# Performance work log

Hardware: AMD Instinct MI355X
Metric: run time of the kernel (lower is better)

The kernel has to match this reference:

```python
import math
import jax, jax.numpy as jnp
import numpy as np

DIM = 1024
HEADS = 16
HEAD_DIM = DIM // HEADS
NEG = -10000.0


def setup_inputs() -> dict:
    key = jax.random.key(0)
    ks = jax.random.split(key, 9)
    B, S = 2, 2048
    s = 1.0 / math.sqrt(DIM)
    inp = {
        "x": jax.random.normal(ks[0], (B, S, DIM), dtype=jnp.float32),
        "Wq": jax.random.normal(ks[1], (DIM, DIM), dtype=jnp.float32) * s,
        "bq": jnp.zeros((DIM,), dtype=jnp.float32),
        "Wk": jax.random.normal(ks[2], (DIM, DIM), dtype=jnp.float32) * s,
        "bk": jnp.zeros((DIM,), dtype=jnp.float32),
        "Wv": jax.random.normal(ks[3], (DIM, DIM), dtype=jnp.float32) * s,
        "bv": jnp.zeros((DIM,), dtype=jnp.float32),
        "Wo": jax.random.normal(ks[4], (DIM, DIM), dtype=jnp.float32) * s,
        "bo": jnp.zeros((DIM,), dtype=jnp.float32),
    }
    return inp


def reference(x, Wq, bq, Wk, bk, Wv, bv, Wo, bo):
    B, S, D = x.shape
    q = x @ Wq + bq
    k = x @ Wk + bk
    v = x @ Wv + bv
    # [B, H, S, hd]
    def split_heads(t):
        return t.reshape(B, S, HEADS, HEAD_DIM).transpose(0, 2, 1, 3)
    q, k, v = split_heads(q), split_heads(k), split_heads(v)
    scores = jnp.einsum("bhqd,bhkd->bhqk", q, k) / math.sqrt(HEAD_DIM)
    causal = jnp.tril(jnp.ones((S, S), dtype=bool))  # [S, S]
    scores = jnp.where(causal[None, None], scores, NEG)
    probs = jax.nn.softmax(scores, axis=-1)
    ctx = jnp.einsum("bhqk,bhkd->bhqd", probs, v)  # [B, H, S, hd]
    ctx = ctx.transpose(0, 2, 1, 3).reshape(B, S, D)
    out = ctx @ Wo + bo
    return out
```

## Files before the change

kernel.cpp:

```cpp
#include <hip/hip_runtime.h>
#include <hip/hip_bf16.h>
#include <math.h>

#define DIMX 1024
#define HEADSX 16
#define HDX 64
#define BBX 2
#define SSX 2048
#define MMX (BBX*SSX)

typedef __bf16 bf16x8 __attribute__((ext_vector_type(8)));
typedef __bf16 bf16x4 __attribute__((ext_vector_type(4)));
typedef float  f32x4  __attribute__((ext_vector_type(4)));

#define NEGF (-1e30f)
#define QSCALE 0.18033688011112042f

template<bool B> struct BoolC { static constexpr bool value = B; };

static __device__ __forceinline__ void gload16(const void* g, void* l) {
  __builtin_amdgcn_global_load_lds(
      (const __attribute__((address_space(1))) unsigned int*)g,
      (__attribute__((address_space(3))) unsigned int*)l, 16, 0, 0);
}

__global__ __launch_bounds__(256) void k_prep(
    const float* __restrict__ x, const float* __restrict__ Wq,
    const float* __restrict__ Wk, const float* __restrict__ Wv,
    const float* __restrict__ Wo, __bf16* __restrict__ xb,
    __bf16* __restrict__ wqkvT, __bf16* __restrict__ woT) {
  const int bid = blockIdx.x;
  if (bid < 4096) {
    int i = (bid * 256 + threadIdx.x) * 4;
    float4 v = *(const float4*)&x[i];
    bf16x4 o = { (__bf16)v.x, (__bf16)v.y, (__bf16)v.z, (__bf16)v.w };
    *(bf16x4*)&xb[i] = o;
    return;
  }
  __shared__ __bf16 tile[64][65];
  const int wb = bid - 4096;
  const int mat = wb >> 8, t8 = wb & 255;
  const float* src = (mat == 0) ? Wq : (mat == 1) ? Wk : (mat == 2) ? Wv : Wo;
  __bf16* dst = (mat < 3) ? (wqkvT + (size_t)mat * DIMX * DIMX) : woT;
  const int tx = t8 & 15, ty = t8 >> 4;
  const int k0 = ty * 64, n0 = tx * 64;
  #pragma unroll
  for (int rep = 0; rep < 16; ++rep) {
    int idx = rep * 256 + threadIdx.x;
    int r = idx >> 6, c = idx & 63;
    tile[r][c] = (__bf16)src[(size_t)(k0 + r) * DIMX + n0 + c];
  }
  __syncthreads();
  #pragma unroll
  for (int rep = 0; rep < 16; ++rep) {
    int idx = rep * 256 + threadIdx.x;
    int r = idx >> 6, c = idx & 63;
    dst[(size_t)(n0 + r) * DIMX + k0 + c] = tile[c][r];
  }
}

__global__ __launch_bounds__(256) void k_gemm_qkv(
    const __bf16* __restrict__ A,
    const __bf16* __restrict__ Bt,
    const float* __restrict__ b0, const float* __restrict__ b1,
    const float* __restrict__ b2,
    __bf16* __restrict__ qb, __bf16* __restrict__ kb, __bf16* __restrict__ vtb) {
  constexpr int BK = 32, K = 1024;
  __shared__ __bf16 As[128 * BK];
  __shared__ __bf16 Bs[128 * BK];
  const int tid = threadIdx.x, lane = tid & 63, wave = tid >> 6;
  const int g = lane >> 4, r16 = lane & 15;
  const int wm = wave & 1, wn = wave >> 1;
  const int id = blockIdx.x;
  const int xcd = id & 7, j96 = id >> 3;
  const int m0 = (xcd * 4 + (j96 & 3)) * 128;
  const int n0 = (j96 >> 2) * 128;

  f32x4 acc[4][4] = {};

  for (int k0 = 0; k0 < K; k0 += BK) {
    __syncthreads();
    #pragma unroll
    for (int i = 0; i < 2; ++i) {
      int c = wave * 64 + lane + 256 * i;
      gload16(&A [(size_t)(m0 + (c >> 2)) * K + k0 + (c & 3) * 8],
              (char*)As + (size_t)(wave * 64 + 256 * i) * 16);
      gload16(&Bt[(size_t)(n0 + (c >> 2)) * K + k0 + (c & 3) * 8],
              (char*)Bs + (size_t)(wave * 64 + 256 * i) * 16);
    }
    __syncthreads();
    bf16x8 af[4], bfr[4];
    #pragma unroll
    for (int i = 0; i < 4; ++i)
      af[i]  = *(const bf16x8*)&As[(wm * 64 + i * 16 + r16) * BK + g * 8];
    #pragma unroll
    for (int j = 0; j < 4; ++j)
      bfr[j] = *(const bf16x8*)&Bs[(wn * 64 + j * 16 + r16) * BK + g * 8];
    #pragma unroll
    for (int i = 0; i < 4; ++i)
      #pragma unroll
      for (int j = 0; j < 4; ++j)
        acc[i][j] = __builtin_amdgcn_mfma_f32_16x16x32_bf16(af[i], bfr[j],
                                                            acc[i][j], 0, 0, 0);
  }

  #pragma unroll
  for (int i = 0; i < 4; ++i) {
    #pragma unroll
    for (int j = 0; j < 4; ++j) {
      #pragma unroll
      for (int r = 0; r < 4; ++r) {
        int m = m0 + wm * 64 + i * 16 + 4 * g + r;
        int n = n0 + wn * 64 + j * 16 + r16;
        float v = acc[i][j][r];
        int proj = n >> 10, w = n & 1023, h = w >> 6, d = w & 63;
        const float* bp = (proj == 0) ? b0 : (proj == 1) ? b1 : b2;
        v += bp[w];
        int b = m >> 11, s = m & 2047, bh = b * HEADSX + h;
        if (proj == 0)      qb [((size_t)bh * SSX + s) * HDX + d] =
                                (__bf16)(v * QSCALE);
        else if (proj == 1) kb [((size_t)bh * SSX + s) * HDX + d] = (__bf16)v;
        else                vtb[((size_t)bh * HDX + d) * SSX + s] = (__bf16)v;
      }
    }
  }
}

__global__ __launch_bounds__(256) void k_gemm_out(
    const __bf16* __restrict__ A,
    const __bf16* __restrict__ Bt,
    const float* __restrict__ bias, float* __restrict__ outf) {
  constexpr int BK = 32, K = 1024;
  __shared__ __bf16 As[128 * BK];
  __shared__ __bf16 Bs[64 * BK];
  const int tid = threadIdx.x, lane = tid & 63, wave = tid >> 6;
  const int g = lane >> 4, r16 = lane & 15;
  const int wm = wave & 1, wn = wave >> 1;
  const int id = blockIdx.x;
  const int xcd = id & 7, j64 = id >> 3;
  const int m0 = (xcd * 4 + (j64 & 3)) * 128;
  const int n0 = (j64 >> 2) * 64;

  f32x4 acc[4][2] = {};

  for (int k0 = 0; k0 < K; k0 += BK) {
    __syncthreads();
    #pragma unroll
    for (int i = 0; i < 2; ++i) {
      int c = wave * 64 + lane + 256 * i;
      gload16(&A [(size_t)(m0 + (c >> 2)) * K + k0 + (c & 3) * 8],
              (char*)As + (size_t)(wave * 64 + 256 * i) * 16);
    }
    {
      int c = tid;
      gload16(&Bt[(size_t)(n0 + (c >> 2)) * K + k0 + (c & 3) * 8],
              (char*)Bs + (size_t)(wave * 64) * 16);
    }
    __syncthreads();
    bf16x8 af[4], bfr[2];
    #pragma unroll
    for (int i = 0; i < 4; ++i)
      af[i]  = *(const bf16x8*)&As[(wm * 64 + i * 16 + r16) * BK + g * 8];
    #pragma unroll
    for (int j = 0; j < 2; ++j)
      bfr[j] = *(const bf16x8*)&Bs[(wn * 32 + j * 16 + r16) * BK + g * 8];
    #pragma unroll
    for (int i = 0; i < 4; ++i)
      #pragma unroll
      for (int j = 0; j < 2; ++j)
        acc[i][j] = __builtin_amdgcn_mfma_f32_16x16x32_bf16(af[i], bfr[j],
                                                            acc[i][j], 0, 0, 0);
  }

  #pragma unroll
  for (int i = 0; i < 4; ++i)
    #pragma unroll
    for (int j = 0; j < 2; ++j)
      #pragma unroll
      for (int r = 0; r < 4; ++r) {
        int m = m0 + wm * 64 + i * 16 + 4 * g + r;
        int n = n0 + wn * 32 + j * 16 + r16;
        outf[(size_t)m * DIMX + n] = acc[i][j][r] + bias[n];
      }
}

__global__ __launch_bounds__(256, 2) void k_attn(
    const __bf16* __restrict__ qb, const __bf16* __restrict__ kb,
    const __bf16* __restrict__ vtb, __bf16* __restrict__ ctxb) {
  const int tid = threadIdx.x;
  const int lane = tid & 63, wq = tid >> 6;
  const int g = lane >> 4, r16 = lane & 15;

  const int id = blockIdx.x;
  const int xcd = id & 7, idx = id >> 3;
  const int bh = xcd * 4 + (idx & 3);
  const int p  = idx >> 2;
  const int b = bh >> 4, h = bh & 15;

  const int ntL = p + 1, ntH = 32 - p;
  const int q0L = p * 64 + wq * 16;
  const int q0H = (31 - p) * 64 + wq * 16;

  const __bf16* Q  = qb  + (size_t)bh * SSX * HDX;
  const __bf16* Kp = kb  + (size_t)bh * SSX * HDX;
  const __bf16* Vt = vtb + (size_t)bh * HDX * SSX;

  __shared__ __bf16 Ks[2][64 * 64];
  __shared__ __bf16 Vs[2][64 * 64];
  __shared__ unsigned Pld[8][512];

  bf16x8 qfL[2], qfH[2];
  qfL[0] = *(const bf16x8*)&Q[(size_t)(q0L + r16) * HDX + g * 8];
  qfL[1] = *(const bf16x8*)&Q[(size_t)(q0L + r16) * HDX + 32 + g * 8];
  qfH[0] = *(const bf16x8*)&Q[(size_t)(q0H + r16) * HDX + g * 8];
  qfH[1] = *(const bf16x8*)&Q[(size_t)(q0H + r16) * HDX + 32 + g * 8];

  f32x4 accL[4] = {}, accH[4] = {};
  float mrunL = NEGF, lrunL = 0.f;
  float mrunH = NEGF, lrunH = 0.f;

  auto STAGE = [&](int buf, int t) {
    const int kv0 = t * 64;
    #pragma unroll
    for (int i = 0; i < 2; ++i) {
      int c = tid + 256 * i;
      int r = c >> 3;
      int cb = (c & 7) ^ (r & 7);
      gload16(&Kp[(size_t)(kv0 + r) * HDX + cb * 8],
              (char*)Ks[buf] + (size_t)(wq * 64 + 256 * i) * 16);
      gload16(&Vt[(size_t)r * SSX + kv0 + cb * 8],
              (char*)Vs[buf] + (size_t)(wq * 64 + 256 * i) * 16);
    }
  };

  auto SM = [&](f32x4* sac, f32x4* acc, float& mrun, float& lrun,
                int qrow, bool last, int kv0, unsigned* pld) {
    float pv[4][4];
    float mt = NEGF;
    #pragma unroll
    for (int jj = 0; jj < 4; ++jj)
      #pragma unroll
      for (int r = 0; r < 4; ++r) {
        float s = sac[jj][r];
        if (last) {
          int kcol = kv0 + jj * 16 + 4 * g + r;
          s = (kcol > qrow) ? NEGF : s;
        }
        pv[jj][r] = s;
        mt = fmaxf(mt, s);
      }
    mt = fmaxf(mt, __shfl_xor(mt, 16));
    mt = fmaxf(mt, __shfl_xor(mt, 32));
    if (__any(mt > mrun)) {
      float mnew = fmaxf(mrun, mt);
      float fac = exp2f(mrun - mnew);
      mrun = mnew;
      lrun *= fac;
      #pragma unroll
      for (int j2 = 0; j2 < 4; ++j2)
        #pragma unroll
        for (int r = 0; r < 4; ++r)
          acc[j2][r] *= fac;
    }
    float rs = 0.f;
    #pragma unroll
    for (int jj = 0; jj < 4; ++jj)
      #pragma unroll
      for (int r = 0; r < 4; ++r) {
        float px = exp2f(pv[jj][r] - mrun);
        pv[jj][r] = px;
        rs += px;
      }
    lrun += rs;
    #pragma unroll
    for (int jj = 0; jj < 4; ++jj)
      #pragma unroll
      for (int rp = 0; rp < 2; ++rp) {
        unsigned w;
        asm("v_cvt_pk_bf16_f32 %0, %1, %2"
            : "=v"(w) : "v"(pv[jj][2 * rp]), "v"(pv[jj][2 * rp + 1]));
        int c = jj * 8 + g * 2 + rp;
        int addr = r16 * 32 + (((c >> 2) ^ (r16 & 7)) << 2) + (c & 3);
        pld[addr] = w;
      }
  };

  auto STEP = [&](auto dolc, int t, bool lastH) {
    constexpr bool doL = decltype(dolc)::value;
    const int cur = t & 1;
    if (t + 1 < ntH) STAGE(cur ^ 1, t + 1);
    const int kv0 = t * 64;

    f32x4 sacH[4] = {}, sacL[4] = {};
    __builtin_amdgcn_s_setprio(1);
    #pragma unroll
    for (int kk = 0; kk < 2; ++kk)
      #pragma unroll
      for (int jj = 0; jj < 4; ++jj) {
        int rr = jj * 16 + r16;
        bf16x8 kf = *(const bf16x8*)
            &Ks[cur][rr * 64 + (((kk << 2) + g) ^ (rr & 7)) * 8];
        sacH[jj] = __builtin_amdgcn_mfma_f32_16x16x32_bf16(kf, qfH[kk],
                                                           sacH[jj], 0, 0, 0);
        if constexpr (doL)
          sacL[jj] = __builtin_amdgcn_mfma_f32_16x16x32_bf16(kf, qfL[kk],
                                                             sacL[jj], 0, 0, 0);
      }
    __builtin_amdgcn_s_setprio(0);

    SM(sacH, accH, mrunH, lrunH, q0H + r16, lastH, kv0, &Pld[wq * 2][0]);
    if constexpr (doL)
      SM(sacL, accL, mrunL, lrunL, q0L + r16, t == ntL - 1, kv0,
         &Pld[wq * 2 + 1][0]);

    bf16x8 pfH[2], pfL[2];
    #pragma unroll
    for (int half = 0; half < 2; ++half) {
      int c = half * 16 + g * 4;
      int addr = r16 * 32 + (((c >> 2) ^ (r16 & 7)) << 2);
      pfH[half] = *(const bf16x8*)&Pld[wq * 2][addr];
      if constexpr (doL) pfL[half] = *(const bf16x8*)&Pld[wq * 2 + 1][addr];
    }
    __builtin_amdgcn_s_setprio(1);
    #pragma unroll
    for (int j2 = 0; j2 < 4; ++j2)
      #pragma unroll
      for (int half = 0; half < 2; ++half) {
        int dd = j2 * 16 + r16;
        bf16x8 vf = *(const bf16x8*)
            &Vs[cur][dd * 64 + (((half << 2) + g) ^ (dd & 7)) * 8];
        accH[j2] = __builtin_amdgcn_mfma_f32_16x16x32_bf16(vf, pfH[half],
                                                           accH[j2], 0, 0, 0);
        if constexpr (doL)
          accL[j2] = __builtin_amdgcn_mfma_f32_16x16x32_bf16(vf, pfL[half],
                                                             accL[j2], 0, 0, 0);
      }
    __builtin_amdgcn_s_setprio(0);
  };

  STAGE(0, 0);
  __syncthreads();

  int t = 0;
  for (; t < ntL; ++t) {
    STEP(BoolC<true>{}, t, false);
    __syncthreads();
  }
  for (; t < ntH; ++t) {
    STEP(BoolC<false>{}, t, t == ntH - 1);
    __syncthreads();
  }

  auto EPIL = [&](f32x4* acc, float lrun, int q0) {
    lrun += __shfl_xor(lrun, 16);
    lrun += __shfl_xor(lrun, 32);
    const float inv = 1.f / lrun;
    const int s = q0 + r16;
    #pragma unroll
    for (int j2 = 0; j2 < 4; ++j2)
      #pragma unroll
      for (int r = 0; r < 4; ++r) {
        int d = j2 * 16 + 4 * g + r;
        ctxb[((size_t)(b * SSX + s)) * DIMX + h * HDX + d] =
            (__bf16)(acc[j2][r] * inv);
      }
  };
  EPIL(accH, lrunH, q0H);
  EPIL(accL, lrunL, q0L);
}

extern "C" void kernel_launch(void* const* d_in, const int* in_sizes, int n_in,
                              void* d_out, int out_size, void* d_ws,
                              size_t ws_size, hipStream_t stream) {
  const float* x  = (const float*)d_in[0];
  const float* Wq = (const float*)d_in[1];
  const float* bq = (const float*)d_in[2];
  const float* Wk = (const float*)d_in[3];
  const float* bk = (const float*)d_in[4];
  const float* Wv = (const float*)d_in[5];
  const float* bv = (const float*)d_in[6];
  const float* Wo = (const float*)d_in[7];
  const float* bo = (const float*)d_in[8];
  float* out = (float*)d_out;

  char* ws = (char*)d_ws;
  __bf16* xb    = (__bf16*)(ws);
  __bf16* wqkvT = (__bf16*)(ws + ((size_t)8  << 20));
  __bf16* woT   = (__bf16*)(ws + ((size_t)14 << 20));
  __bf16* qb    = (__bf16*)(ws + ((size_t)16 << 20));
  __bf16* kb    = (__bf16*)(ws + ((size_t)24 << 20));
  __bf16* vtb   = (__bf16*)(ws + ((size_t)32 << 20));
  __bf16* ctxb  = xb;

  k_prep<<<5120, 256, 0, stream>>>(x, Wq, Wk, Wv, Wo, xb, wqkvT, woT);
  k_gemm_qkv<<<768, 256, 0, stream>>>(xb, wqkvT, bq, bk, bv, qb, kb, vtb);
  k_attn<<<512, 256, 0, stream>>>(qb, kb, vtb, ctxb);
  k_gemm_out<<<512, 256, 0, stream>>>(ctxb, woT, bo, out);
}
```

Before: 117.5 us.

## Split attention low/high query tiles across 8 waves and widen GEMM K-tile

The attention kernel now runs 512 threads per block. Waves 0-3 handle the high (long) query tile and waves 4-7 handle the paired low tile, so each wave holds one accumulator set instead of two. This lowers register pressure and raises parallelism, at the cost of the low-tile waves idling at barriers once their shorter causal range is done. Both GEMMs move to BK=64 with XOR-swizzled LDS layouts, which halves the barrier count per K loop and avoids bank conflicts.

```diff
diff --git a/kernel.cpp b/kernel.cpp
--- a/kernel.cpp
+++ b/kernel.cpp
@@ -15,8 +15,6 @@
 
 #define NEGF (-1e30f)
 #define QSCALE 0.18033688011112042f
-
-template<bool B> struct BoolC { static constexpr bool value = B; };
 
 static __device__ __forceinline__ void gload16(const void* g, void* l) {
   __builtin_amdgcn_global_load_lds(
@@ -65,7 +63,7 @@
     const float* __restrict__ b0, const float* __restrict__ b1,
     const float* __restrict__ b2,
     __bf16* __restrict__ qb, __bf16* __restrict__ kb, __bf16* __restrict__ vtb) {
-  constexpr int BK = 32, K = 1024;
+  constexpr int BK = 64, K = 1024;
   __shared__ __bf16 As[128 * BK];
   __shared__ __bf16 Bs[128 * BK];
   const int tid = threadIdx.x, lane = tid & 63, wave = tid >> 6;
@@ -81,27 +79,35 @@
   for (int k0 = 0; k0 < K; k0 += BK) {
     __syncthreads();
     #pragma unroll
-    for (int i = 0; i < 2; ++i) {
-      int c = wave * 64 + lane + 256 * i;
-      gload16(&A [(size_t)(m0 + (c >> 2)) * K + k0 + (c & 3) * 8],
+    for (int i = 0; i < 4; ++i) {
+      int c = tid + 256 * i;
+      int r = c >> 3, cb = (c & 7) ^ (r & 7);
+      gload16(&A [(size_t)(m0 + r) * K + k0 + cb * 8],
               (char*)As + (size_t)(wave * 64 + 256 * i) * 16);
-      gload16(&Bt[(size_t)(n0 + (c >> 2)) * K + k0 + (c & 3) * 8],
+      gload16(&Bt[(size_t)(n0 + r) * K + k0 + cb * 8],
               (char*)Bs + (size_t)(wave * 64 + 256 * i) * 16);
     }
     __syncthreads();
-    bf16x8 af[4], bfr[4];
-    #pragma unroll
-    for (int i = 0; i < 4; ++i)
-      af[i]  = *(const bf16x8*)&As[(wm * 64 + i * 16 + r16) * BK + g * 8];
-    #pragma unroll
-    for (int j = 0; j < 4; ++j)
-      bfr[j] = *(const bf16x8*)&Bs[(wn * 64 + j * 16 + r16) * BK + g * 8];
-    #pragma unroll
-    for (int i = 0; i < 4; ++i)
-      #pragma unroll
-      for (int j = 0; j < 4; ++j)
-        acc[i][j] = __builtin_amdgcn_mfma_f32_16x16x32_bf16(af[i], bfr[j],
-                                                            acc[i][j], 0, 0, 0);
+    #pragma unroll
+    for (int kk = 0; kk < 2; ++kk) {
+      bf16x8 af[4], bfr[4];
+      #pragma unroll
+      for (int i = 0; i < 4; ++i) {
+        int rr = wm * 64 + i * 16 + r16;
+        af[i] = *(const bf16x8*)&As[rr * 64 + (((kk << 2) + g) ^ (rr & 7)) * 8];
+      }
+      #pragma unroll
+      for (int j = 0; j < 4; ++j) {
+        int rn = wn * 64 + j * 16 + r16;
+        bfr[j] = *(const bf16x8*)&Bs[rn * 64 + (((kk << 2) + g) ^ (rn & 7)) * 8];
+      }
+      #pragma unroll
+      for (int i = 0; i < 4; ++i)
+        #pragma unroll
+        for (int j = 0; j < 4; ++j)
+          acc[i][j] = __builtin_amdgcn_mfma_f32_16x16x32_bf16(af[i], bfr[j],
+                                                              acc[i][j], 0, 0, 0);
+    }
   }
 
   #pragma unroll
@@ -130,7 +136,7 @@
     const __bf16* __restrict__ A,
     const __bf16* __restrict__ Bt,
     const float* __restrict__ bias, float* __restrict__ outf) {
-  constexpr int BK = 32, K = 1024;
+  constexpr int BK = 64, K = 1024;
   __shared__ __bf16 As[128 * BK];
   __shared__ __bf16 Bs[64 * BK];
   const int tid = threadIdx.x, lane = tid & 63, wave = tid >> 6;
@@ -146,30 +152,40 @@
   for (int k0 = 0; k0 < K; k0 += BK) {
     __syncthreads();
     #pragma unroll
+    for (int i = 0; i < 4; ++i) {
+      int c = tid + 256 * i;
+      int r = c >> 3, cb = (c & 7) ^ (r & 7);
+      gload16(&A[(size_t)(m0 + r) * K + k0 + cb * 8],
+              (char*)As + (size_t)(wave * 64 + 256 * i) * 16);
+    }
+    #pragma unroll
     for (int i = 0; i < 2; ++i) {
-      int c = wave * 64 + lane + 256 * i;
-      gload16(&A [(size_t)(m0 + (c >> 2)) * K + k0 + (c & 3) * 8],
-              (char*)As + (size_t)(wave * 64 + 256 * i) * 16);
-    }
-    {
-      int c = tid;
-      gload16(&Bt[(size_t)(n0 + (c >> 2)) * K + k0 + (c & 3) * 8],
-              (char*)Bs + (size_t)(wave * 64) * 16);
-    }
-    __syncthreads();
-    bf16x8 af[4], bfr[2];
-    #pragma unroll
-    for (int i = 0; i < 4; ++i)
-      af[i]  = *(const bf16x8*)&As[(wm * 64 + i * 16 + r16) * BK + g * 8];
-    #pragma unroll
-    for (int j = 0; j < 2; ++j)
-      bfr[j] = *(const bf16x8*)&Bs[(wn * 32 + j * 16 + r16) * BK + g * 8];
-    #pragma unroll
-    for (int i = 0; i < 4; ++i)
-      #pragma unroll
-      for (int j = 0; j < 2; ++j)
-        acc[i][j] = __builtin_amdgcn_mfma_f32_16x16x32_bf16(af[i], bfr[j],
-                                                            acc[i][j], 0, 0, 0);
+      int c = tid + 256 * i;
+      int r = c >> 3, cb = (c & 7) ^ (r & 7);
+      gload16(&Bt[(size_t)(n0 + r) * K + k0 + cb * 8],
+              (char*)Bs + (size_t)(wave * 64 + 256 * i) * 16);
+    }
+    __syncthreads();
+    #pragma unroll
+    for (int kk = 0; kk < 2; ++kk) {
+      bf16x8 af[4], bfr[2];
+      #pragma unroll
+      for (int i = 0; i < 4; ++i) {
+        int rr = wm * 64 + i * 16 + r16;
+        af[i] = *(const bf16x8*)&As[rr * 64 + (((kk << 2) + g) ^ (rr & 7)) * 8];
+      }
+      #pragma unroll
+      for (int j = 0; j < 2; ++j) {
+        int rn = wn * 32 + j * 16 + r16;
+        bfr[j] = *(const bf16x8*)&Bs[rn * 64 + (((kk << 2) + g) ^ (rn & 7)) * 8];
+      }
+      #pragma unroll
+      for (int i = 0; i < 4; ++i)
+        #pragma unroll
+        for (int j = 0; j < 2; ++j)
+          acc[i][j] = __builtin_amdgcn_mfma_f32_16x16x32_bf16(af[i], bfr[j],
+                                                              acc[i][j], 0, 0, 0);
+    }
   }
 
   #pragma unroll
@@ -184,7 +200,7 @@
       }
 }
 
-__global__ __launch_bounds__(256, 2) void k_attn(
+__global__ __launch_bounds__(512, 4) void k_attn(
     const __bf16* __restrict__ qb, const __bf16* __restrict__ kb,
     const __bf16* __restrict__ vtb, __bf16* __restrict__ ctxb) {
   const int tid = threadIdx.x;
@@ -198,8 +214,10 @@
   const int b = bh >> 4, h = bh & 15;
 
   const int ntL = p + 1, ntH = 32 - p;
-  const int q0L = p * 64 + wq * 16;
-  const int q0H = (31 - p) * 64 + wq * 16;
+  const bool isH = (wq < 4);
+  const int myNt = isH ? ntH : ntL;
+  const int q0 = isH ? ((31 - p) * 64 + wq * 16)
+                     : (p * 64 + (wq - 4) * 16);
 
   const __bf16* Q  = qb  + (size_t)bh * SSX * HDX;
   const __bf16* Kp = kb  + (size_t)bh * SSX * HDX;
@@ -209,164 +227,135 @@
   __shared__ __bf16 Vs[2][64 * 64];
   __shared__ unsigned Pld[8][512];
 
-  bf16x8 qfL[2], qfH[2];
-  qfL[0] = *(const bf16x8*)&Q[(size_t)(q0L + r16) * HDX + g * 8];
-  qfL[1] = *(const bf16x8*)&Q[(size_t)(q0L + r16) * HDX + 32 + g * 8];
-  qfH[0] = *(const bf16x8*)&Q[(size_t)(q0H + r16) * HDX + g * 8];
-  qfH[1] = *(const bf16x8*)&Q[(size_t)(q0H + r16) * HDX + 32 + g * 8];
-
-  f32x4 accL[4] = {}, accH[4] = {};
-  float mrunL = NEGF, lrunL = 0.f;
-  float mrunH = NEGF, lrunH = 0.f;
+  bf16x8 qf[2];
+  qf[0] = *(const bf16x8*)&Q[(size_t)(q0 + r16) * HDX + g * 8];
+  qf[1] = *(const bf16x8*)&Q[(size_t)(q0 + r16) * HDX + 32 + g * 8];
+
+  f32x4 acc[4] = {};
+  float mrun = NEGF, lrun = 0.f;
+  const int qrow = q0 + r16;
 
   auto STAGE = [&](int buf, int t) {
     const int kv0 = t * 64;
-    #pragma unroll
-    for (int i = 0; i < 2; ++i) {
-      int c = tid + 256 * i;
-      int r = c >> 3;
-      int cb = (c & 7) ^ (r & 7);
-      gload16(&Kp[(size_t)(kv0 + r) * HDX + cb * 8],
-              (char*)Ks[buf] + (size_t)(wq * 64 + 256 * i) * 16);
-      gload16(&Vt[(size_t)r * SSX + kv0 + cb * 8],
-              (char*)Vs[buf] + (size_t)(wq * 64 + 256 * i) * 16);
-    }
+    int c = tid;
+    int r = c >> 3;
+    int cb = (c & 7) ^ (r & 7);
+    gload16(&Kp[(size_t)(kv0 + r) * HDX + cb * 8],
+            (char*)Ks[buf] + (size_t)(wq * 64) * 16);
+    gload16(&Vt[(size_t)r * SSX + kv0 + cb * 8],
+            (char*)Vs[buf] + (size_t)(wq * 64) * 16);
   };
 
-  auto SM = [&](f32x4* sac, f32x4* acc, float& mrun, float& lrun,
-                int qrow, bool last, int kv0, unsigned* pld) {
-    float pv[4][4];
-    float mt = NEGF;
-    #pragma unroll
-    for (int jj = 0; jj < 4; ++jj)
-      #pragma unroll
-      for (int r = 0; r < 4; ++r) {
-        float s = sac[jj][r];
-        if (last) {
-          int kcol = kv0 + jj * 16 + 4 * g + r;
-          s = (kcol > qrow) ? NEGF : s;
-        }
-        pv[jj][r] = s;
-        mt = fmaxf(mt, s);
-      }
-    mt = fmaxf(mt, __shfl_xor(mt, 16));
-    mt = fmaxf(mt, __shfl_xor(mt, 32));
-    if (__any(mt > mrun)) {
-      float mnew = fmaxf(mrun, mt);
-      float fac = exp2f(mrun - mnew);
-      mrun = mnew;
-      lrun *= fac;
-      #pragma unroll
-      for (int j2 = 0; j2 < 4; ++j2)
-        #pragma unroll
-        for (int r = 0; r < 4; ++r)
-          acc[j2][r] *= fac;
-    }
-    float rs = 0.f;
-    #pragma unroll
-    for (int jj = 0; jj < 4; ++jj)
-      #pragma unroll
-      for (int r = 0; r < 4; ++r) {
-        float px = exp2f(pv[jj][r] - mrun);
-        pv[jj][r] = px;
-        rs += px;
-      }
-    lrun += rs;
-    #pragma unroll
-    for (int jj = 0; jj < 4; ++jj)
-      #pragma unroll
-      for (int rp = 0; rp < 2; ++rp) {
-        unsigned w;
-        asm("v_cvt_pk_bf16_f32 %0, %1, %2"
-            : "=v"(w) : "v"(pv[jj][2 * rp]), "v"(pv[jj][2 * rp + 1]));
-        int c = jj * 8 + g * 2 + rp;
-        int addr = r16 * 32 + (((c >> 2) ^ (r16 & 7)) << 2) + (c & 3);
-        pld[addr] = w;
-      }
-  };
-
-  auto STEP = [&](auto dolc, int t, bool lastH) {
-    constexpr bool doL = decltype(dolc)::value;
+  STAGE(0, 0);
+  __syncthreads();
+
+  for (int t = 0; t < ntH; ++t) {
     const int cur = t & 1;
     if (t + 1 < ntH) STAGE(cur ^ 1, t + 1);
-    const int kv0 = t * 64;
-
-    f32x4 sacH[4] = {}, sacL[4] = {};
-    __builtin_amdgcn_s_setprio(1);
-    #pragma unroll
-    for (int kk = 0; kk < 2; ++kk)
-      #pragma unroll
-      for (int jj = 0; jj < 4; ++jj) {
-        int rr = jj * 16 + r16;
-        bf16x8 kf = *(const bf16x8*)
-            &Ks[cur][rr * 64 + (((kk << 2) + g) ^ (rr & 7)) * 8];
-        sacH[jj] = __builtin_amdgcn_mfma_f32_16x16x32_bf16(kf, qfH[kk],
-                                                           sacH[jj], 0, 0, 0);
-        if constexpr (doL)
-          sacL[jj] = __builtin_amdgcn_mfma_f32_16x16x32_bf16(kf, qfL[kk],
-                                                             sacL[jj], 0, 0, 0);
-      }
-    __builtin_amdgcn_s_setprio(0);
-
-    SM(sacH, accH, mrunH, lrunH, q0H + r16, lastH, kv0, &Pld[wq * 2][0]);
-    if constexpr (doL)
-      SM(sacL, accL, mrunL, lrunL, q0L + r16, t == ntL - 1, kv0,
-         &Pld[wq * 2 + 1][0]);
-
-    bf16x8 pfH[2], pfL[2];
-    #pragma unroll
-    for (int half = 0; half < 2; ++half) {
-      int c = half * 16 + g * 4;
-      int addr = r16 * 32 + (((c >> 2) ^ (r16 & 7)) << 2);
-      pfH[half] = *(const bf16x8*)&Pld[wq * 2][addr];
-      if constexpr (doL) pfL[half] = *(const bf16x8*)&Pld[wq * 2 + 1][addr];
-    }
-    __builtin_amdgcn_s_setprio(1);
-    #pragma unroll
-    for (int j2 = 0; j2 < 4; ++j2)
+    if (t < myNt) {
+      const int kv0 = t * 64;
+      const bool last = (t == myNt - 1);
+
+      f32x4 sac[4] = {};
+      __builtin_amdgcn_s_setprio(1);
+      #pragma unroll
+      for (int kk = 0; kk < 2; ++kk)
+        #pragma unroll
+        for (int jj = 0; jj < 4; ++jj) {
+          int rr = jj * 16 + r16;
+          bf16x8 kf = *(const bf16x8*)
+              &Ks[cur][rr * 64 + (((kk << 2) + g) ^ (rr & 7)) * 8];
+          sac[jj] = __builtin_amdgcn_mfma_f32_16x16x32_bf16(kf, qf[kk],
+                                                            sac[jj], 0, 0, 0);
+        }
+      __builtin_amdgcn_s_setprio(0);
+
+      float pv[4][4];
+      float mt = NEGF;
+      #pragma unroll
+      for (int jj = 0; jj < 4; ++jj)
+        #pragma unroll
+        for (int r = 0; r < 4; ++r) {
+          float s = sac[jj][r];
+          if (last) {
+            int kcol = kv0 + jj * 16 + 4 * g + r;
+            s = (kcol > qrow) ? NEGF : s;
+          }
+          pv[jj][r] = s;
+          mt = fmaxf(mt, s);
+        }
+      mt = fmaxf(mt, __shfl_xor(mt, 16));
+      mt = fmaxf(mt, __shfl_xor(mt, 32));
+
+      if (__any(mt > mrun)) {
+        float mnew = fmaxf(mrun, mt);
+        float fac = exp2f(mrun - mnew);
+        mrun = mnew;
+        lrun *= fac;
+        #pragma unroll
+        for (int j2 = 0; j2 < 4; ++j2)
+          #pragma unroll
+          for (int r = 0; r < 4; ++r)
+            acc[j2][r] *= fac;
+      }
+      float rs = 0.f;
+      #pragma unroll
+      for (int jj = 0; jj < 4; ++jj)
+        #pragma unroll
+        for (int r = 0; r < 4; ++r) {
+          float px = exp2f(pv[jj][r] - mrun);
+          pv[jj][r] = px;
+          rs += px;
+        }
+      lrun += rs;
+
+      #pragma unroll
+      for (int jj = 0; jj < 4; ++jj)
+        #pragma unroll
+        for (int rp = 0; rp < 2; ++rp) {
+          unsigned w;
+          asm("v_cvt_pk_bf16_f32 %0, %1, %2"
+              : "=v"(w) : "v"(pv[jj][2 * rp]), "v"(pv[jj][2 * rp + 1]));
+          int c = jj * 8 + g * 2 + rp;
+          int addr = r16 * 32 + (((c >> 2) ^ (r16 & 7)) << 2) + (c & 3);
+          Pld[wq][addr] = w;
+        }
+
+      bf16x8 pf[2];
       #pragma unroll
       for (int half = 0; half < 2; ++half) {
-        int dd = j2 * 16 + r16;
-        bf16x8 vf = *(const bf16x8*)
-            &Vs[cur][dd * 64 + (((half << 2) + g) ^ (dd & 7)) * 8];
-        accH[j2] = __builtin_amdgcn_mfma_f32_16x16x32_bf16(vf, pfH[half],
-                                                           accH[j2], 0, 0, 0);
-        if constexpr (doL)
-          accL[j2] = __builtin_amdgcn_mfma_f32_16x16x32_bf16(vf, pfL[half],
-                                                             accL[j2], 0, 0, 0);
-      }
-    __builtin_amdgcn_s_setprio(0);
-  };
-
-  STAGE(0, 0);
-  __syncthreads();
-
-  int t = 0;
-  for (; t < ntL; ++t) {
-    STEP(BoolC<true>{}, t, false);
-    __syncthreads();
-  }
-  for (; t < ntH; ++t) {
-    STEP(BoolC<false>{}, t, t == ntH - 1);
-    __syncthreads();
-  }
-
-  auto EPIL = [&](f32x4* acc, float lrun, int q0) {
-    lrun += __shfl_xor(lrun, 16);
-    lrun += __shfl_xor(lrun, 32);
-    const float inv = 1.f / lrun;
-    const int s = q0 + r16;
-    #pragma unroll
-    for (int j2 = 0; j2 < 4; ++j2)
-      #pragma unroll
-      for (int r = 0; r < 4; ++r) {
-        int d = j2 * 16 + 4 * g + r;
-        ctxb[((size_t)(b * SSX + s)) * DIMX + h * HDX + d] =
-            (__bf16)(acc[j2][r] * inv);
-      }
-  };
-  EPIL(accH, lrunH, q0H);
-  EPIL(accL, lrunL, q0L);
+        int c = half * 16 + g * 4;
+        int addr = r16 * 32 + (((c >> 2) ^ (r16 & 7)) << 2);
+        pf[half] = *(const bf16x8*)&Pld[wq][addr];
+      }
+      __builtin_amdgcn_s_setprio(1);
+      #pragma unroll
+      for (int j2 = 0; j2 < 4; ++j2)
+        #pragma unroll
+        for (int half = 0; half < 2; ++half) {
+          int dd = j2 * 16 + r16;
+          bf16x8 vf = *(const bf16x8*)
+              &Vs[cur][dd * 64 + (((half << 2) + g) ^ (dd & 7)) * 8];
+          acc[j2] = __builtin_amdgcn_mfma_f32_16x16x32_bf16(vf, pf[half],
+                                                            acc[j2], 0, 0, 0);
+        }
+      __builtin_amdgcn_s_setprio(0);
+    }
+    __syncthreads();
+  }
+
+  lrun += __shfl_xor(lrun, 16);
+  lrun += __shfl_xor(lrun, 32);
+  const float inv = 1.f / lrun;
+  const int s = q0 + r16;
+  #pragma unroll
+  for (int j2 = 0; j2 < 4; ++j2)
+    #pragma unroll
+    for (int r = 0; r < 4; ++r) {
+      int d = j2 * 16 + 4 * g + r;
+      ctxb[((size_t)(b * SSX + s)) * DIMX + h * HDX + d] =
+          (__bf16)(acc[j2][r] * inv);
+    }
 }
 
 extern "C" void kernel_launch(void* const* d_in, const int* in_sizes, int n_in,
@@ -394,6 +383,6 @@
 
   k_prep<<<5120, 256, 0, stream>>>(x, Wq, Wk, Wv, Wo, xb, wqkvT, woT);
   k_gemm_qkv<<<768, 256, 0, stream>>>(xb, wqkvT, bq, bk, bv, qb, kb, vtb);
-  k_attn<<<512, 256, 0, stream>>>(qb, kb, vtb, ctxb);
+  k_attn<<<512, 512, 0, stream>>>(qb, kb, vtb, ctxb);
   k_gemm_out<<<512, 256, 0, stream>>>(ctxb, woT, bo, out);
 }
```

After: 128.5 us. +9.4%, slower.

## Process two KV tiles per barrier with four-slot LDS ring buffer

Applied to the files above, without the earlier changes.

The attention loop now stages K/V into a four-slot LDS ring and handles two 64-key tiles per iteration, so there is one __syncthreads per two tiles and prefetch runs two tiles ahead. The interleaved low/high query-tile MFMA issue is replaced by sequential per-subtile processing that shares one P scratch buffer per wave. This cuts barrier count and increases load lookahead, at the cost of doubling K/V LDS use (fewer resident blocks) and losing the interleaving of independent L/H MFMA chains.

```diff
diff --git a/kernel.cpp b/kernel.cpp
--- a/kernel.cpp
+++ b/kernel.cpp
@@ -15,8 +15,6 @@
 
 #define NEGF (-1e30f)
 #define QSCALE 0.18033688011112042f
-
-template<bool B> struct BoolC { static constexpr bool value = B; };
 
 static __device__ __forceinline__ void gload16(const void* g, void* l) {
   __builtin_amdgcn_global_load_lds(
@@ -205,9 +203,9 @@
   const __bf16* Kp = kb  + (size_t)bh * SSX * HDX;
   const __bf16* Vt = vtb + (size_t)bh * HDX * SSX;
 
-  __shared__ __bf16 Ks[2][64 * 64];
-  __shared__ __bf16 Vs[2][64 * 64];
-  __shared__ unsigned Pld[8][512];
+  __shared__ __bf16 Ks[4][64 * 64];
+  __shared__ __bf16 Vs[4][64 * 64];
+  __shared__ unsigned Pld[4][512];
 
   bf16x8 qfL[2], qfH[2];
   qfL[0] = *(const bf16x8*)&Q[(size_t)(q0L + r16) * HDX + g * 8];
@@ -219,7 +217,8 @@
   float mrunL = NEGF, lrunL = 0.f;
   float mrunH = NEGF, lrunH = 0.f;
 
-  auto STAGE = [&](int buf, int t) {
+  auto STAGE = [&](int t) {
+    const int slot = t & 3;
     const int kv0 = t * 64;
     #pragma unroll
     for (int i = 0; i < 2; ++i) {
@@ -227,14 +226,28 @@
       int r = c >> 3;
       int cb = (c & 7) ^ (r & 7);
       gload16(&Kp[(size_t)(kv0 + r) * HDX + cb * 8],
-              (char*)Ks[buf] + (size_t)(wq * 64 + 256 * i) * 16);
+              (char*)Ks[slot] + (size_t)(wq * 64 + 256 * i) * 16);
       gload16(&Vt[(size_t)r * SSX + kv0 + cb * 8],
-              (char*)Vs[buf] + (size_t)(wq * 64 + 256 * i) * 16);
+              (char*)Vs[slot] + (size_t)(wq * 64 + 256 * i) * 16);
     }
   };
 
-  auto SM = [&](f32x4* sac, f32x4* acc, float& mrun, float& lrun,
-                int qrow, bool last, int kv0, unsigned* pld) {
+  auto SUBTILE = [&](const bf16x8* qf, f32x4* acc, float& mrun, float& lrun,
+                     int qrow, bool last, int kv0, int slot) {
+    f32x4 sac[4] = {};
+    __builtin_amdgcn_s_setprio(1);
+    #pragma unroll
+    for (int kk = 0; kk < 2; ++kk)
+      #pragma unroll
+      for (int jj = 0; jj < 4; ++jj) {
+        int rr = jj * 16 + r16;
+        bf16x8 kf = *(const bf16x8*)
+            &Ks[slot][rr * 64 + (((kk << 2) + g) ^ (rr & 7)) * 8];
+        sac[jj] = __builtin_amdgcn_mfma_f32_16x16x32_bf16(kf, qf[kk], sac[jj],
+                                                          0, 0, 0);
+      }
+    __builtin_amdgcn_s_setprio(0);
+
     float pv[4][4];
     float mt = NEGF;
     #pragma unroll
@@ -251,6 +264,7 @@
       }
     mt = fmaxf(mt, __shfl_xor(mt, 16));
     mt = fmaxf(mt, __shfl_xor(mt, 32));
+
     if (__any(mt > mrun)) {
       float mnew = fmaxf(mrun, mt);
       float fac = exp2f(mrun - mnew);
@@ -272,6 +286,7 @@
         rs += px;
       }
     lrun += rs;
+
     #pragma unroll
     for (int jj = 0; jj < 4; ++jj)
       #pragma unroll
@@ -281,45 +296,15 @@
             : "=v"(w) : "v"(pv[jj][2 * rp]), "v"(pv[jj][2 * rp + 1]));
         int c = jj * 8 + g * 2 + rp;
         int addr = r16 * 32 + (((c >> 2) ^ (r16 & 7)) << 2) + (c & 3);
-        pld[addr] = w;
-      }
-  };
-
-  auto STEP = [&](auto dolc, int t, bool lastH) {
-    constexpr bool doL = decltype(dolc)::value;
-    const int cur = t & 1;
-    if (t + 1 < ntH) STAGE(cur ^ 1, t + 1);
-    const int kv0 = t * 64;
-
-    f32x4 sacH[4] = {}, sacL[4] = {};
-    __builtin_amdgcn_s_setprio(1);
-    #pragma unroll
-    for (int kk = 0; kk < 2; ++kk)
-      #pragma unroll
-      for (int jj = 0; jj < 4; ++jj) {
-        int rr = jj * 16 + r16;
-        bf16x8 kf = *(const bf16x8*)
-            &Ks[cur][rr * 64 + (((kk << 2) + g) ^ (rr & 7)) * 8];
-        sacH[jj] = __builtin_amdgcn_mfma_f32_16x16x32_bf16(kf, qfH[kk],
-                                                           sacH[jj], 0, 0, 0);
-        if constexpr (doL)
-          sacL[jj] = __builtin_amdgcn_mfma_f32_16x16x32_bf16(kf, qfL[kk],
-                                                             sacL[jj], 0, 0, 0);
-      }
-    __builtin_amdgcn_s_setprio(0);
-
-    SM(sacH, accH, mrunH, lrunH, q0H + r16, lastH, kv0, &Pld[wq * 2][0]);
-    if constexpr (doL)
-      SM(sacL, accL, mrunL, lrunL, q0L + r16, t == ntL - 1, kv0,
-         &Pld[wq * 2 + 1][0]);
-
-    bf16x8 pfH[2], pfL[2];
+        Pld[wq][addr] = w;
+      }
+
+    bf16x8 pf[2];
     #pragma unroll
     for (int half = 0; half < 2; ++half) {
       int c = half * 16 + g * 4;
       int addr = r16 * 32 + (((c >> 2) ^ (r16 & 7)) << 2);
-      pfH[half] = *(const bf16x8*)&Pld[wq * 2][addr];
-      if constexpr (doL) pfL[half] = *(const bf16x8*)&Pld[wq * 2 + 1][addr];
+      pf[half] = *(const bf16x8*)&Pld[wq][addr];
     }
     __builtin_amdgcn_s_setprio(1);
     #pragma unroll
@@ -328,26 +313,32 @@
       for (int half = 0; half < 2; ++half) {
         int dd = j2 * 16 + r16;
         bf16x8 vf = *(const bf16x8*)
-            &Vs[cur][dd * 64 + (((half << 2) + g) ^ (dd & 7)) * 8];
-        accH[j2] = __builtin_amdgcn_mfma_f32_16x16x32_bf16(vf, pfH[half],
-                                                           accH[j2], 0, 0, 0);
-        if constexpr (doL)
-          accL[j2] = __builtin_amdgcn_mfma_f32_16x16x32_bf16(vf, pfL[half],
-                                                             accL[j2], 0, 0, 0);
+            &Vs[slot][dd * 64 + (((half << 2) + g) ^ (dd & 7)) * 8];
+        acc[j2] = __builtin_amdgcn_mfma_f32_16x16x32_bf16(vf, pf[half],
+                                                          acc[j2], 0, 0, 0);
       }
     __builtin_amdgcn_s_setprio(0);
   };
 
-  STAGE(0, 0);
+  STAGE(0);
+  if (ntH > 1) STAGE(1);
   __syncthreads();
 
-  int t = 0;
-  for (; t < ntL; ++t) {
-    STEP(BoolC<true>{}, t, false);
-    __syncthreads();
-  }
-  for (; t < ntH; ++t) {
-    STEP(BoolC<false>{}, t, t == ntH - 1);
+  for (int t = 0; t < ntH; t += 2) {
+    if (t + 2 < ntH) STAGE(t + 2);
+    if (t + 3 < ntH) STAGE(t + 3);
+
+    SUBTILE(qfH, accH, mrunH, lrunH, q0H + r16, t == ntH - 1, t * 64, t & 3);
+    if (t < ntL)
+      SUBTILE(qfL, accL, mrunL, lrunL, q0L + r16, t == ntL - 1, t * 64, t & 3);
+
+    if (t + 1 < ntH) {
+      SUBTILE(qfH, accH, mrunH, lrunH, q0H + r16, t + 1 == ntH - 1,
+              (t + 1) * 64, (t + 1) & 3);
+      if (t + 1 < ntL)
+        SUBTILE(qfL, accL, mrunL, lrunL, q0L + r16, t + 1 == ntL - 1,
+                (t + 1) * 64, (t + 1) & 3);
+    }
     __syncthreads();
   }
 
```

Result: slower. 120.7 us (+2.7%).
